# Kernel optimization log

Hardware: AMD Instinct MI355X
Metric: run time of the kernel (lower is better)

## Reference

```python
import jax, jax.numpy as jnp
import numpy as np

B, NPG, DEG = 512, 128, 16          # graphs, nodes/graph, out-degree
N = B * NPG                          # 65536 nodes
E = N * DEG                          # 1048576 edges
IN_DIM, HID, HEADS = 11, 32, 4
K1 = int(np.ceil(0.8 * NPG))         # 103 nodes/graph after pool1
K2 = int(np.ceil(0.8 * K1))          # 83 nodes/graph after pool2


def gat_conv(x, src, dst, mask, W, a_s, a_d, b, n_nodes):
    # PyG GATConv (concat=True, add_self_loops=True, eval mode -> no dropout)
    xp = (x @ W).reshape(n_nodes, HEADS, HID)            # [N,H,C]
    as_ = jnp.einsum('nhc,hc->nh', xp, a_s)
    ad_ = jnp.einsum('nhc,hc->nh', xp, a_d)
    loop = jnp.arange(n_nodes)
    s = jnp.concatenate([src, loop])
    d = jnp.concatenate([dst, loop])
    m = jnp.concatenate([mask, jnp.ones(n_nodes, bool)])
    logit = jax.nn.leaky_relu(as_[s] + ad_[d], 0.2)      # [E+N,H]
    logit = jnp.where(m[:, None], logit, -1e9)
    mx = jax.ops.segment_max(logit, d, num_segments=n_nodes)
    ex = jnp.exp(logit - mx[d]) * m[:, None]
    den = jax.ops.segment_sum(ex, d, num_segments=n_nodes)
    alpha = ex / (den[d] + 1e-16)                        # segment softmax over dst
    out = jax.ops.segment_sum(alpha[:, :, None] * xp[s], d, num_segments=n_nodes)
    return out.reshape(n_nodes, HEADS * HID) + b


def topk_pool(x, src, dst, mask, w, npg, k):
    # PyG TopKPooling: score = tanh((x*w).sum(-1)/||w||); keep top ceil(ratio*n) per graph
    nb = x.shape[0] // npg
    score = jnp.tanh((x @ w) / jnp.linalg.norm(w))
    vals, idx = jax.lax.top_k(score.reshape(nb, npg), k)  # [B,k]
    perm = (idx + (jnp.arange(nb) * npg)[:, None]).reshape(-1)
    x_new = x[perm] * vals.reshape(-1, 1)
    remap = jnp.full(nb * npg, -1).at[perm].set(jnp.arange(nb * k))
    ns, nd = remap[src], remap[dst]
    m = mask & (ns >= 0) & (nd >= 0)
    return x_new, jnp.where(m, ns, 0), jnp.where(m, nd, 0), m


def setup_inputs():
    key = jax.random.key(0)
    ks = jax.random.split(key, 24)
    s = 0.05
    x = jax.random.normal(ks[0], (N, IN_DIM), jnp.float32)
    src = jnp.repeat(jnp.arange(N), DEG)
    dst = (src // NPG) * NPG + jax.random.randint(ks[1], (E,), 0, NPG)
    edge_index = jnp.stack([src, dst])
    edge_attr = jax.random.normal(ks[2], (E, 4), jnp.float32)
    batch = jnp.repeat(jnp.arange(B), NPG)
    p = dict(
        W_g1=jax.random.normal(ks[3], (IN_DIM, HEADS * HID), jnp.float32) * s,
        att_src1=jax.random.normal(ks[4], (HEADS, HID), jnp.float32) * s,
        att_dst1=jax.random.normal(ks[5], (HEADS, HID), jnp.float32) * s,
        b_g1=jnp.zeros((HEADS * HID,), jnp.float32),
        W_t1=jax.random.normal(ks[6], (HEADS * HID, HID), jnp.float32) * s,
        b_t1=jnp.zeros((HID,), jnp.float32),
        pool_w1=jax.random.normal(ks[7], (HID,), jnp.float32) * s,
        W_g2=jax.random.normal(ks[8], (HID, HEADS * HID), jnp.float32) * s,
        att_src2=jax.random.normal(ks[9], (HEADS, HID), jnp.float32) * s,
        att_dst2=jax.random.normal(ks[10], (HEADS, HID), jnp.float32) * s,
        b_g2=jnp.zeros((HEADS * HID,), jnp.float32),
        W_t2=jax.random.normal(ks[11], (HEADS * HID, HID), jnp.float32) * s,
        b_t2=jnp.zeros((HID,), jnp.float32),
        pool_w2=jax.random.normal(ks[12], (HID,), jnp.float32) * s,
        W_l1=jax.random.normal(ks[13], (2 * HID, 256), jnp.float32) * s,
        b_l1=jnp.zeros((256,), jnp.float32),
        W_l2=jax.random.normal(ks[14], (256, 1024), jnp.float32) * s,
        b_l2=jnp.zeros((1024,), jnp.float32),
        W_l3=jax.random.normal(ks[15], (1024, 1), jnp.float32) * s,
        b_l3=jnp.zeros((1,), jnp.float32),
    )
    return dict(x=x, edge_index=edge_index, edge_attr=edge_attr, batch=batch, **p)


def reference(x, edge_index, edge_attr, batch,
              W_g1, att_src1, att_dst1, b_g1, W_t1, b_t1, pool_w1,
              W_g2, att_src2, att_dst2, b_g2, W_t2, b_t2, pool_w2,
              W_l1, b_l1, W_l2, b_l2, W_l3, b_l3):
    # edge_attr is ignored (GATConv built without edge_dim); batch is implicit
    # in the fixed equal-size graph layout.  Eval mode -> dropout disabled.
    src, dst = edge_index[0], edge_index[1]
    mask = jnp.ones(E, bool)
    h = jax.nn.relu(gat_conv(x, src, dst, mask, W_g1, att_src1, att_dst1, b_g1, N))
    h = h @ W_t1 + b_t1
    h, src, dst, mask = topk_pool(h, src, dst, mask, pool_w1, NPG, K1)
    h1 = h.reshape(B, K1, HID)
    g1 = jnp.concatenate([h1.max(1), h1.mean(1)], axis=1)   # [B, 2*HID]
    h = jax.nn.relu(gat_conv(h, src, dst, mask, W_g2, att_src2, att_dst2, b_g2, B * K1))
    h = h @ W_t2 + b_t2
    h, src, dst, mask = topk_pool(h, src, dst, mask, pool_w2, K1, K2)
    h2 = h.reshape(B, K2, HID)
    g2 = jnp.concatenate([h2.max(1), h2.mean(1)], axis=1)
    g = g1 + g2
    g = jax.nn.relu(g @ W_l1 + b_l1)
    g = jax.nn.relu(g @ W_l2 + b_l2)
    return g @ W_l3 + b_l3                                   # [B,1]
```

## Files before the change

### kernel.cpp

```cpp
#include <hip/hip_runtime.h>
#include <math.h>

constexpr int NPGc  = 128;
constexpr int NG    = 512;
constexpr int EPGc  = 2048;
constexpr int ETOT  = 1048576;
constexpr int IND   = 11;
constexpr int HIDc  = 32;
constexpr int FD    = 128;
constexpr int K1c   = 103;
constexpr int K2c   = 83;
constexpr int NN    = NG * NPGc;
constexpr int N2c   = NG * K1c;

__device__ __forceinline__ float lrelu(float x){ return fmaxf(x, 0.2f*x); }

template<int KIN>
__device__ void foldDev(const float* __restrict__ Wg, const float* __restrict__ avs,
                        const float* __restrict__ avd, float* __restrict__ S, float* __restrict__ D, int t)
{
    if (t < KIN * 4) {
        int k = t >> 2, h = t & 3;
        float s = 0.f, d = 0.f;
        for (int j = 0; j < HIDc; j++) {
            float w = Wg[k*FD + h*HIDc + j];
            s = fmaf(w, avs[h*HIDc + j], s);
            d = fmaf(w, avd[h*HIDc + j], d);
        }
        S[t] = s; D[t] = d;
    }
}

__global__ __launch_bounds__(256) void k_prep(const int* __restrict__ ei,
    const float* __restrict__ W1g, const float* __restrict__ s1, const float* __restrict__ d1,
    const float* __restrict__ W2g, const float* __restrict__ s2, const float* __restrict__ d2,
    int* __restrict__ csrOff, unsigned char* __restrict__ csrSB,
    float* __restrict__ S1, float* __restrict__ D1, float* __restrict__ S2, float* __restrict__ D2)
{
    int b = blockIdx.x, t = threadIdx.x;
    if (b >= NG) {
        if (b == NG)     foldDev<IND>(W1g, s1, d1, S1, D1, t);
        else             foldDev<HIDc>(W2g, s2, d2, S2, D2, t);
        return;
    }
    int g = b;
    __shared__ int cnt[128], cur[128], offL[129];
    __shared__ unsigned char sbL[EPGc];
    if (t < 128) cnt[t] = 0;
    __syncthreads();
    const int* dstG = ei + ETOT + g * EPGc;
    int dnv[8];
    #pragma unroll
    for (int q = 0; q < 8; q++) {
        int e = t + 256*q;
        dnv[q] = dstG[e] - g * NPGc;
        atomicAdd(&cnt[dnv[q]], 1);
    }
    __syncthreads();
    if (t < 64) {
        int c0 = cnt[2*t], c1 = cnt[2*t + 1], ps = c0 + c1, P = ps;
        #pragma unroll
        for (int dl = 1; dl < 64; dl <<= 1) { int v = __shfl_up(P, dl); if (t >= dl) P += v; }
        int E0 = P - ps;
        offL[2*t] = E0; offL[2*t + 1] = E0 + c0;
        cur[2*t]  = E0; cur[2*t + 1]  = E0 + c0;
        if (t == 63) offL[128] = P;
    }
    __syncthreads();
    #pragma unroll
    for (int q = 0; q < 8; q++) {
        int e = t + 256*q;
        int pos = atomicAdd(&cur[dnv[q]], 1);
        sbL[pos] = (unsigned char)(e >> 4);
    }
    __syncthreads();
    if (t < 128) ((int4*)(csrSB + (size_t)g * EPGc))[t] = ((const int4*)sbL)[t];
    if (t <= NPGc) csrOff[g*132 + t] = offL[t];
}

template<int NNODE, int KIN>
__global__ __launch_bounds__(256) void k_gat(
    const float* __restrict__ xin, const float* __restrict__ Wg,
    const float* __restrict__ WsS, const float* __restrict__ WsD,
    const int* __restrict__ csrOff, const unsigned char* __restrict__ csrSB,
    const float* __restrict__ bias, const float* __restrict__ Wt,
    float* __restrict__ htp)
{
    int g = blockIdx.x, h = blockIdx.y, t = threadIdx.x;
    constexpr int UN = (NNODE*KIN > EPGc ? NNODE*KIN : EPGc);
    __shared__ __align__(16) float xpL[NNODE * 36];
    __shared__ __align__(16) float uni[UN];
    __shared__ __align__(16) unsigned char sbL[EPGc];
    __shared__ float asL[NNODE], adL[NNODE], sfW[NNODE], sDen[NNODE];
    __shared__ int offL[NNODE + 1];
    __shared__ float WL[KIN * 32];
    __shared__ float WsSL[KIN], WsDL[KIN], bL[32];
    __shared__ __align__(16) float WtsL[1024];

    float* xF  = uni;
    float* wEL = uni;

    {
        const float* xg = xin + (size_t)g * NNODE * KIN;
        if constexpr ((KIN & 3) == 0) {
            for (int i = t; i < NNODE * (KIN/4); i += 256)
                ((float4*)xF)[i] = ((const float4*)xg)[i];
        } else {
            for (int i = t; i < NNODE * KIN; i += 256) xF[i] = xg[i];
        }
    }
    for (int i = t; i < KIN * 32; i += 256) { int k = i >> 5, c = i & 31; WL[i] = Wg[k*FD + h*32 + c]; }
    if (t < KIN) { WsSL[t] = WsS[t*4 + h]; WsDL[t] = WsD[t*4 + h]; }
    if (t < 32) bL[t] = bias[h*32 + t];
    if (t <= NNODE) offL[t] = csrOff[g*132 + t];
    if (t < 128) ((int4*)sbL)[t] = ((const int4*)(csrSB + (size_t)g * EPGc))[t];
    ((float4*)WtsL)[t] = ((const float4*)(Wt + h*1024))[t];
    __syncthreads();

    for (int p = t; p < NNODE * 32; p += 256) {
        int n = p >> 5, c = p & 31;
        const float* xr = xF + n * KIN;
        float acc = 0.f;
        #pragma unroll
        for (int k = 0; k < KIN; k++) acc = fmaf(xr[k], WL[k*32 + c], acc);
        xpL[n*36 + c] = acc;
    }
    if (t < NNODE) {
        const float* xr = xF + t * KIN;
        float s = 0.f, d = 0.f;
        #pragma unroll
        for (int k = 0; k < KIN; k++) { float v = xr[k]; s = fmaf(v, WsSL[k], s); d = fmaf(v, WsDL[k], d); }
        asL[t] = s; adL[t] = d;
    }
    __syncthreads();

    if (t < NNODE) {
        float as_n = asL[t], adn = adL[t];
        int lo = offL[t], hi = offL[t + 1];
        float mx = as_n;
        for (int i = lo; i < hi; i++) mx = fmaxf(mx, asL[sbL[i]]);
        float m = lrelu(mx + adn);
        float ws = expf(lrelu(as_n + adn) - m);
        float den = ws;
        for (int i = lo; i < hi; i++) {
            float w = expf(lrelu(asL[sbL[i]] + adn) - m);
            wEL[i] = w; den += w;
        }
        sfW[t] = ws; sDen[t] = den;
    }
    __syncthreads();

    const float4* X4 = (const float4*)xpL;
    float4 rv[4];
    #pragma unroll
    for (int r = 0; r < 4; r++) {
        int p = t + r*256;
        if (p < NNODE * 8) {
            int n = p >> 3, c4 = p & 7;
            float w0 = sfW[n];
            float4 v = X4[n*9 + c4];
            float4 a; a.x = w0*v.x; a.y = w0*v.y; a.z = w0*v.z; a.w = w0*v.w;
            int lo = offL[n], hi = offL[n + 1];
            for (int s = lo; s < hi; s++) {
                int sc = sbL[s]; float w = wEL[s];
                float4 u = X4[sc*9 + c4];
                a.x = fmaf(w, u.x, a.x); a.y = fmaf(w, u.y, a.y);
                a.z = fmaf(w, u.z, a.z); a.w = fmaf(w, u.w, a.w);
            }
            float inv = 1.f / (sDen[n] + 1e-16f);
            rv[r].x = fmaxf(fmaf(a.x, inv, bL[c4*4 + 0]), 0.f);
            rv[r].y = fmaxf(fmaf(a.y, inv, bL[c4*4 + 1]), 0.f);
            rv[r].z = fmaxf(fmaf(a.z, inv, bL[c4*4 + 2]), 0.f);
            rv[r].w = fmaxf(fmaf(a.w, inv, bL[c4*4 + 3]), 0.f);
        }
    }
    __syncthreads();
    {
        float4* X4w = (float4*)xpL;
        #pragma unroll
        for (int r = 0; r < 4; r++) {
            int p = t + r*256;
            if (p < NNODE * 8) X4w[(p>>3)*9 + (p&7)] = rv[r];
        }
    }
    __syncthreads();

    const int n0 = t >> 3, j4 = t & 7;
    float4 a0 = make_float4(0,0,0,0), a1 = a0, a2 = a0, a3 = a0;
    #pragma unroll 8
    for (int c = 0; c < 32; c++) {
        float4 w4 = *(const float4*)&WtsL[c*HIDc + j4*4];
        float r0 = xpL[n0*36 + c];
        a0.x = fmaf(r0, w4.x, a0.x); a0.y = fmaf(r0, w4.y, a0.y);
        a0.z = fmaf(r0, w4.z, a0.z); a0.w = fmaf(r0, w4.w, a0.w);
        if (n0 + 32 < NNODE) {
            float r1 = xpL[(n0+32)*36 + c];
            a1.x = fmaf(r1, w4.x, a1.x); a1.y = fmaf(r1, w4.y, a1.y);
            a1.z = fmaf(r1, w4.z, a1.z); a1.w = fmaf(r1, w4.w, a1.w);
        }
        if (n0 + 64 < NNODE) {
            float r2 = xpL[(n0+64)*36 + c];
            a2.x = fmaf(r2, w4.x, a2.x); a2.y = fmaf(r2, w4.y, a2.y);
            a2.z = fmaf(r2, w4.z, a2.z); a2.w = fmaf(r2, w4.w, a2.w);
        }
        if (n0 + 96 < NNODE) {
            float r3 = xpL[(n0+96)*36 + c];
            a3.x = fmaf(r3, w4.x, a3.x); a3.y = fmaf(r3, w4.y, a3.y);
            a3.z = fmaf(r3, w4.z, a3.z); a3.w = fmaf(r3, w4.w, a3.w);
        }
    }
    {
        size_t base = ((size_t)(g * NNODE + n0) * 4 + h) * 32 + j4 * 4;
        *(float4*)(htp + base) = a0;
        if (n0 + 32 < NNODE) *(float4*)(htp + base + (size_t)32*128) = a1;
        if (n0 + 64 < NNODE) *(float4*)(htp + base + (size_t)64*128) = a2;
        if (n0 + 96 < NNODE) *(float4*)(htp + base + (size_t)96*128) = a3;
    }
}

template<int NIN, int KEEP, bool FIRST>
__global__ __launch_bounds__(256) void k_linpool(
    const float* __restrict__ htp, const float* __restrict__ bt, const float* __restrict__ pw,
    float* __restrict__ xnew, const int* __restrict__ ei,
    int* __restrict__ csrOffW, unsigned char* __restrict__ sbW,
    float* __restrict__ gfeat, const float* __restrict__ gprev,
    const float* __restrict__ W1, const float* __restrict__ b1,
    const float* __restrict__ W2, const float* __restrict__ b2,
    const float* __restrict__ W3, const float* __restrict__ b3,
    float* __restrict__ outp)
{
    int g = blockIdx.x, t = threadIdx.x;
    __shared__ float htL[NIN * 33];
    __shared__ float scoreL[NIN];
    __shared__ int rnkL[NIN];
    __shared__ int cnt[128], cur[128], offL[129];
    __shared__ unsigned char sbL[EPGc];
    __shared__ float gvec[64];
    __shared__ float h1L[256], red[256];

    for (int p = t; p < NIN * 8; p += 256) {
        int n = p >> 3, q = p & 7;
        const float4* row = (const float4*)(htp + (size_t)(g * NIN + n) * 128);
        float4 s = ((const float4*)bt)[q];
        float4 p0 = row[q], p1 = row[8 + q], p2 = row[16 + q], p3 = row[24 + q];
        s.x += p0.x; s.y += p0.y; s.z += p0.z; s.w += p0.w;
        s.x += p1.x; s.y += p1.y; s.z += p1.z; s.w += p1.w;
        s.x += p2.x; s.y += p2.y; s.z += p2.z; s.w += p2.w;
        s.x += p3.x; s.y += p3.y; s.z += p3.z; s.w += p3.w;
        float* d = htL + n*33 + q*4;
        d[0] = s.x; d[1] = s.y; d[2] = s.z; d[3] = s.w;
    }
    __syncthreads();

    float nrm; { float ss = 0.f; for (int k = 0; k < HIDc; k++) { float w = pw[k]; ss = fmaf(w, w, ss); } nrm = sqrtf(ss); }
    if (t < NIN) {
        float dot = 0.f;
        for (int k = 0; k < HIDc; k++) dot = fmaf(htL[t*33 + k], pw[k], dot);
        scoreL[t] = tanhf(dot / nrm);
    }
    __syncthreads();
    if (t < NIN) {
        float si = scoreL[t]; int rank = 0;
        for (int q = 0; q < NIN; q++) {
            float sj = scoreL[q];
            rank += (sj > si || (sj == si && q < t)) ? 1 : 0;
        }
        rnkL[t] = (rank < KEEP) ? rank : -1;
    }
    __syncthreads();
    if constexpr (FIRST) {
        for (int p = t; p < NIN * 32; p += 256) {
            int n = p >> 5, jj = p & 31;
            int rk = rnkL[n];
            if (rk >= 0) xnew[((size_t)g*KEEP + rk)*HIDc + jj] = htL[n*33 + jj] * scoreL[n];
        }
    }
    if (t < HIDc) {
        float mx = -INFINITY, sm = 0.f;
        for (int n = 0; n < NIN; n++) {
            if (rnkL[n] >= 0) { float v = htL[n*33 + t] * scoreL[n]; mx = fmaxf(mx, v); sm += v; }
        }
        float mean = sm / (float)KEEP;
        if constexpr (FIRST) {
            gfeat[(size_t)g*64 + t]      = mx;
            gfeat[(size_t)g*64 + 32 + t] = mean;
        } else {
            gvec[t]      = gprev[(size_t)g*64 + t] + mx;
            gvec[32 + t] = gprev[(size_t)g*64 + 32 + t] + mean;
        }
    }

    if constexpr (FIRST) {
        __syncthreads();
        if (t < 128) cnt[t] = 0;
        __syncthreads();
        const int* dstG = ei + ETOT + g * EPGc;
        int snv[8], dnv[8];
        #pragma unroll
        for (int q = 0; q < 8; q++) {
            int e = t + 256*q;
            int s = rnkL[e >> 4], d = rnkL[dstG[e] - g * NPGc];
            bool ok = (s >= 0 && d >= 0);
            snv[q] = s; dnv[q] = ok ? d : -1;
            if (ok) atomicAdd(&cnt[d], 1);
        }
        __syncthreads();
        if (t < 64) {
            int c0 = cnt[2*t], c1 = cnt[2*t + 1], ps = c0 + c1, P = ps;
            #pragma unroll
            for (int dl = 1; dl < 64; dl <<= 1) { int v = __shfl_up(P, dl); if (t >= dl) P += v; }
            int E0 = P - ps;
            offL[2*t] = E0; offL[2*t + 1] = E0 + c0;
            cur[2*t]  = E0; cur[2*t + 1]  = E0 + c0;
            if (t == 63) offL[128] = P;
        }
        __syncthreads();
        #pragma unroll
        for (int q = 0; q < 8; q++) {
            if (dnv[q] >= 0) {
                int pos = atomicAdd(&cur[dnv[q]], 1);
                sbL[pos] = (unsigned char)snv[q];
            }
        }
        __syncthreads();
        if (t < 128) ((int4*)(sbW + (size_t)g * EPGc))[t] = ((const int4*)sbL)[t];
        if (t <= K1c) csrOffW[g*132 + t] = offL[t];
    } else {
        __syncthreads();
        float a = b1[t];
        #pragma unroll 4
        for (int k = 0; k < 64; k++) a = fmaf(gvec[k], W1[k*256 + t], a);
        h1L[t] = fmaxf(a, 0.f);
        __syncthreads();
        float c0 = b2[t], c1 = b2[t + 256], c2 = b2[t + 512], c3 = b2[t + 768];
        const float* w2c = W2 + t;
        #pragma unroll 4
        for (int i = 0; i < 256; i++) {
            float hv = h1L[i];
            const float* wr = w2c + (size_t)i * 1024;
            c0 = fmaf(hv, wr[0],   c0);
            c1 = fmaf(hv, wr[256], c1);
            c2 = fmaf(hv, wr[512], c2);
            c3 = fmaf(hv, wr[768], c3);
        }
        float p = fmaf(fmaxf(c0, 0.f), W3[t],
                  fmaf(fmaxf(c1, 0.f), W3[t + 256],
                  fmaf(fmaxf(c2, 0.f), W3[t + 512],
                       fmaxf(c3, 0.f) * W3[t + 768])));
        red[t] = p;
        __syncthreads();
        for (int s = 128; s > 0; s >>= 1) { if (t < s) red[t] += red[t + s]; __syncthreads(); }
        if (t == 0) outp[g] = red[0] + b3[0];
    }
}

extern "C" void kernel_launch(void* const* d_in, const int* in_sizes, int n_in,
                              void* d_out, int out_size, void* d_ws, size_t ws_size,
                              hipStream_t stream)
{
    const float* x    = (const float*)d_in[0];
    const int*   ei   = (const int*)  d_in[1];
    const float* W_g1 = (const float*)d_in[4];
    const float* as1w = (const float*)d_in[5];
    const float* ad1w = (const float*)d_in[6];
    const float* b_g1 = (const float*)d_in[7];
    const float* W_t1 = (const float*)d_in[8];
    const float* b_t1 = (const float*)d_in[9];
    const float* pw1  = (const float*)d_in[10];
    const float* W_g2 = (const float*)d_in[11];
    const float* as2w = (const float*)d_in[12];
    const float* ad2w = (const float*)d_in[13];
    const float* b_g2 = (const float*)d_in[14];
    const float* W_t2 = (const float*)d_in[15];
    const float* b_t2 = (const float*)d_in[16];
    const float* pw2  = (const float*)d_in[17];
    const float* W_l1 = (const float*)d_in[18];
    const float* b_l1 = (const float*)d_in[19];
    const float* W_l2 = (const float*)d_in[20];
    const float* b_l2 = (const float*)d_in[21];
    const float* W_l3 = (const float*)d_in[22];
    const float* b_l3 = (const float*)d_in[23];
    float* out = (float*)d_out;

    char* ws = (char*)d_ws;
    size_t off = 0;
    auto alloc = [&](size_t bytes) -> void* {
        void* p = (void*)(ws + off);
        off += ((bytes + 255) / 256) * 256;
        return p;
    };
    float* htp1  = (float*)alloc((size_t)NN * 128 * 4);
    float* htp2  = (float*)alloc((size_t)N2c * 128 * 4);
    float* x2    = (float*)alloc((size_t)N2c * HIDc * 4);
    float* g1    = (float*)alloc((size_t)NG * 64 * 4);
    float* wsS1  = (float*)alloc(64 * 4);
    float* wsD1  = (float*)alloc(64 * 4);
    float* wsS2  = (float*)alloc(128 * 4);
    float* wsD2  = (float*)alloc(128 * 4);
    int*   off1  = (int*)  alloc((size_t)NG * 132 * 4);
    unsigned char* sb1 = (unsigned char*)alloc((size_t)NG * EPGc);
    int*   off2  = (int*)  alloc((size_t)NG * 132 * 4);
    unsigned char* sb2 = (unsigned char*)alloc((size_t)NG * EPGc);

    k_prep<<<NG + 2, 256, 0, stream>>>(ei, W_g1, as1w, ad1w, W_g2, as2w, ad2w,
                                       off1, sb1, wsS1, wsD1, wsS2, wsD2);

    k_gat<NPGc, IND><<<dim3(NG, 4), 256, 0, stream>>>(
        x, W_g1, wsS1, wsD1, off1, sb1, b_g1, W_t1, htp1);

    k_linpool<NPGc, K1c, true><<<NG, 256, 0, stream>>>(
        htp1, b_t1, pw1, x2, ei, off2, sb2, g1, nullptr,
        nullptr, nullptr, nullptr, nullptr, nullptr, nullptr, nullptr);

    k_gat<K1c, HIDc><<<dim3(NG, 4), 256, 0, stream>>>(
        x2, W_g2, wsS2, wsD2, off2, sb2, b_g2, W_t2, htp2);

    k_linpool<K1c, K2c, false><<<NG, 256, 0, stream>>>(
        htp2, b_t2, pw2, nullptr, nullptr, nullptr, nullptr, nullptr, g1,
        W_l1, b_l1, W_l2, b_l2, W_l3, b_l3, out);
}
```

Baseline: 299.0 us.

## Pad CSR rows to 4, swizzle LDS features, and unroll GAT gathers

After: 622.7 us. 2.08x slower.

```diff
diff --git a/kernel.cpp b/kernel.cpp
--- a/kernel.cpp
+++ b/kernel.cpp
@@ -12,6 +12,9 @@
 constexpr int K2c   = 83;
 constexpr int NN    = NG * NPGc;
 constexpr int N2c   = NG * K1c;
+constexpr int EPAD  = 2432;
+constexpr int SBCAP = 2560;
+constexpr int OFFSTR= 264;
 
 __device__ __forceinline__ float lrelu(float x){ return fmaxf(x, 0.2f*x); }
 
@@ -45,8 +48,9 @@
     }
     int g = b;
     __shared__ int cnt[128], cur[128], offL[129];
-    __shared__ unsigned char sbL[EPGc];
+    __shared__ __align__(16) unsigned char sbL[SBCAP];
     if (t < 128) cnt[t] = 0;
+    if (t < SBCAP/16) ((int4*)sbL)[t] = make_int4(0,0,0,0);
     __syncthreads();
     const int* dstG = ei + ETOT + g * EPGc;
     int dnv[8];
@@ -58,12 +62,14 @@
     }
     __syncthreads();
     if (t < 64) {
-        int c0 = cnt[2*t], c1 = cnt[2*t + 1], ps = c0 + c1, P = ps;
+        int c0 = cnt[2*t], c1 = cnt[2*t + 1];
+        int p0 = (c0 + 3) & ~3, p1 = (c1 + 3) & ~3;
+        int ps = p0 + p1, P = ps;
         #pragma unroll
         for (int dl = 1; dl < 64; dl <<= 1) { int v = __shfl_up(P, dl); if (t >= dl) P += v; }
         int E0 = P - ps;
-        offL[2*t] = E0; offL[2*t + 1] = E0 + c0;
-        cur[2*t]  = E0; cur[2*t + 1]  = E0 + c0;
+        offL[2*t] = E0; offL[2*t + 1] = E0 + p0;
+        cur[2*t]  = E0; cur[2*t + 1]  = E0 + p0;
         if (t == 63) offL[128] = P;
     }
     __syncthreads();
@@ -74,12 +80,13 @@
         sbL[pos] = (unsigned char)(e >> 4);
     }
     __syncthreads();
-    if (t < 128) ((int4*)(csrSB + (size_t)g * EPGc))[t] = ((const int4*)sbL)[t];
-    if (t <= NPGc) csrOff[g*132 + t] = offL[t];
+    if (t < SBCAP/16) ((int4*)(csrSB + (size_t)g * SBCAP))[t] = ((const int4*)sbL)[t];
+    if (t <= 128) csrOff[g*OFFSTR + t] = offL[t];
+    if (t < 128)  csrOff[g*OFFSTR + 132 + t] = cur[t];
 }
 
 template<int NNODE, int KIN>
-__global__ __launch_bounds__(256) void k_gat(
+__global__ __launch_bounds__(256, 5) void k_gat(
     const float* __restrict__ xin, const float* __restrict__ Wg,
     const float* __restrict__ WsS, const float* __restrict__ WsD,
     const int* __restrict__ csrOff, const unsigned char* __restrict__ csrSB,
@@ -87,43 +94,45 @@
     float* __restrict__ htp)
 {
     int g = blockIdx.x, h = blockIdx.y, t = threadIdx.x;
-    constexpr int UN = (NNODE*KIN > EPGc ? NNODE*KIN : EPGc);
-    __shared__ __align__(16) float xpL[NNODE * 36];
+    constexpr int UN = (NNODE*KIN > EPAD ? NNODE*KIN : EPAD);
+    __shared__ __align__(16) float xpL[NNODE * 32];
     __shared__ __align__(16) float uni[UN];
-    __shared__ __align__(16) unsigned char sbL[EPGc];
+    __shared__ __align__(16) unsigned char sbL[SBCAP];
     __shared__ float asL[NNODE], adL[NNODE], sfW[NNODE], sDen[NNODE];
-    __shared__ int offL[NNODE + 1];
-    __shared__ float WL[KIN * 32];
+    __shared__ unsigned short offL[NNODE + 1], endL[NNODE];
     __shared__ float WsSL[KIN], WsDL[KIN], bL[32];
-    __shared__ __align__(16) float WtsL[1024];
 
     float* xF  = uni;
     float* wEL = uni;
 
+    float wcol[KIN];
+    {
+        const float* wg = Wg + h*32 + (t & 31);
+        #pragma unroll
+        for (int k = 0; k < KIN; k++) wcol[k] = wg[k*FD];
+    }
     {
         const float* xg = xin + (size_t)g * NNODE * KIN;
-        if constexpr ((KIN & 3) == 0) {
-            for (int i = t; i < NNODE * (KIN/4); i += 256)
-                ((float4*)xF)[i] = ((const float4*)xg)[i];
-        } else {
-            for (int i = t; i < NNODE * KIN; i += 256) xF[i] = xg[i];
-        }
-    }
-    for (int i = t; i < KIN * 32; i += 256) { int k = i >> 5, c = i & 31; WL[i] = Wg[k*FD + h*32 + c]; }
+        constexpr int XF4 = NNODE * KIN / 4;
+        for (int i = t; i < XF4; i += 256) ((float4*)xF)[i] = ((const float4*)xg)[i];
+    }
     if (t < KIN) { WsSL[t] = WsS[t*4 + h]; WsDL[t] = WsD[t*4 + h]; }
     if (t < 32) bL[t] = bias[h*32 + t];
-    if (t <= NNODE) offL[t] = csrOff[g*132 + t];
-    if (t < 128) ((int4*)sbL)[t] = ((const int4*)(csrSB + (size_t)g * EPGc))[t];
-    ((float4*)WtsL)[t] = ((const float4*)(Wt + h*1024))[t];
-    __syncthreads();
-
-    for (int p = t; p < NNODE * 32; p += 256) {
-        int n = p >> 5, c = p & 31;
-        const float* xr = xF + n * KIN;
-        float acc = 0.f;
-        #pragma unroll
-        for (int k = 0; k < KIN; k++) acc = fmaf(xr[k], WL[k*32 + c], acc);
-        xpL[n*36 + c] = acc;
+    if (t <= NNODE) offL[t] = (unsigned short)csrOff[g*OFFSTR + t];
+    if (t < NNODE)  endL[t] = (unsigned short)csrOff[g*OFFSTR + 132 + t];
+    if (t < SBCAP/16) ((int4*)sbL)[t] = ((const int4*)(csrSB + (size_t)g * SBCAP))[t];
+    __syncthreads();
+
+    {
+        const int c = t & 31, r0 = t >> 5;
+        const int c4v = c >> 2, csw = c & 3;
+        for (int r = r0; r < NNODE; r += 8) {
+            const float* xr = xF + r * KIN;
+            float acc = 0.f;
+            #pragma unroll
+            for (int k = 0; k < KIN; k++) acc = fmaf(xr[k], wcol[k], acc);
+            xpL[r*32 + (((c4v ^ (r & 7)) << 2) | csw)] = acc;
+        }
     }
     if (t < NNODE) {
         const float* xr = xF + t * KIN;
@@ -136,16 +145,34 @@
 
     if (t < NNODE) {
         float as_n = asL[t], adn = adL[t];
-        int lo = offL[t], hi = offL[t + 1];
+        int lo = offL[t], er = endL[t], hp = offL[t + 1];
         float mx = as_n;
-        for (int i = lo; i < hi; i++) mx = fmaxf(mx, asL[sbL[i]]);
+        int i = lo;
+        for (; i + 4 <= er; i += 4) {
+            unsigned int q4 = *(const unsigned int*)(sbL + i);
+            float a0 = asL[q4 & 255], a1 = asL[(q4 >> 8) & 255];
+            float a2 = asL[(q4 >> 16) & 255], a3 = asL[q4 >> 24];
+            mx = fmaxf(fmaxf(fmaxf(fmaxf(mx, a0), a1), a2), a3);
+        }
+        for (; i < er; i++) mx = fmaxf(mx, asL[sbL[i]]);
         float m = lrelu(mx + adn);
         float ws = expf(lrelu(as_n + adn) - m);
         float den = ws;
-        for (int i = lo; i < hi; i++) {
+        i = lo;
+        for (; i + 4 <= er; i += 4) {
+            unsigned int q4 = *(const unsigned int*)(sbL + i);
+            float w0 = expf(lrelu(asL[q4 & 255] + adn) - m);
+            float w1 = expf(lrelu(asL[(q4 >> 8) & 255] + adn) - m);
+            float w2 = expf(lrelu(asL[(q4 >> 16) & 255] + adn) - m);
+            float w3 = expf(lrelu(asL[q4 >> 24] + adn) - m);
+            *(float4*)(wEL + i) = make_float4(w0, w1, w2, w3);
+            den += w0; den += w1; den += w2; den += w3;
+        }
+        for (; i < er; i++) {
             float w = expf(lrelu(asL[sbL[i]] + adn) - m);
             wEL[i] = w; den += w;
         }
+        for (; i < hp; i++) wEL[i] = 0.f;
         sfW[t] = ws; sDen[t] = den;
     }
     __syncthreads();
@@ -158,14 +185,24 @@
         if (p < NNODE * 8) {
             int n = p >> 3, c4 = p & 7;
             float w0 = sfW[n];
-            float4 v = X4[n*9 + c4];
+            float4 v = X4[n*8 + (c4 ^ (n & 7))];
             float4 a; a.x = w0*v.x; a.y = w0*v.y; a.z = w0*v.z; a.w = w0*v.w;
             int lo = offL[n], hi = offL[n + 1];
-            for (int s = lo; s < hi; s++) {
-                int sc = sbL[s]; float w = wEL[s];
-                float4 u = X4[sc*9 + c4];
-                a.x = fmaf(w, u.x, a.x); a.y = fmaf(w, u.y, a.y);
-                a.z = fmaf(w, u.z, a.z); a.w = fmaf(w, u.w, a.w);
+            for (int s = lo; s < hi; s += 4) {
+                unsigned int q4 = *(const unsigned int*)(sbL + s);
+                float4 w4 = *(const float4*)(wEL + s);
+                int s0 = q4 & 255;         float4 u0 = X4[s0*8 + (c4 ^ (s0 & 7))];
+                a.x = fmaf(w4.x, u0.x, a.x); a.y = fmaf(w4.x, u0.y, a.y);
+                a.z = fmaf(w4.x, u0.z, a.z); a.w = fmaf(w4.x, u0.w, a.w);
+                int s1 = (q4 >> 8) & 255;  float4 u1 = X4[s1*8 + (c4 ^ (s1 & 7))];
+                a.x = fmaf(w4.y, u1.x, a.x); a.y = fmaf(w4.y, u1.y, a.y);
+                a.z = fmaf(w4.y, u1.z, a.z); a.w = fmaf(w4.y, u1.w, a.w);
+                int s2 = (q4 >> 16) & 255; float4 u2 = X4[s2*8 + (c4 ^ (s2 & 7))];
+                a.x = fmaf(w4.z, u2.x, a.x); a.y = fmaf(w4.z, u2.y, a.y);
+                a.z = fmaf(w4.z, u2.z, a.z); a.w = fmaf(w4.z, u2.w, a.w);
+                int s3 = q4 >> 24;         float4 u3 = X4[s3*8 + (c4 ^ (s3 & 7))];
+                a.x = fmaf(w4.w, u3.x, a.x); a.y = fmaf(w4.w, u3.y, a.y);
+                a.z = fmaf(w4.w, u3.z, a.z); a.w = fmaf(w4.w, u3.w, a.w);
             }
             float inv = 1.f / (sDen[n] + 1e-16f);
             rv[r].x = fmaxf(fmaf(a.x, inv, bL[c4*4 + 0]), 0.f);
@@ -180,33 +217,40 @@
         #pragma unroll
         for (int r = 0; r < 4; r++) {
             int p = t + r*256;
-            if (p < NNODE * 8) X4w[(p>>3)*9 + (p&7)] = rv[r];
+            if (p < NNODE * 8) {
+                int n = p >> 3, c4 = p & 7;
+                X4w[n*8 + (c4 ^ (n & 7))] = rv[r];
+            }
         }
     }
     __syncthreads();
 
     const int n0 = t >> 3, j4 = t & 7;
+    const float* WtH = Wt + h*1024 + j4*4;
     float4 a0 = make_float4(0,0,0,0), a1 = a0, a2 = a0, a3 = a0;
-    #pragma unroll 8
-    for (int c = 0; c < 32; c++) {
-        float4 w4 = *(const float4*)&WtsL[c*HIDc + j4*4];
-        float r0 = xpL[n0*36 + c];
-        a0.x = fmaf(r0, w4.x, a0.x); a0.y = fmaf(r0, w4.y, a0.y);
-        a0.z = fmaf(r0, w4.z, a0.z); a0.w = fmaf(r0, w4.w, a0.w);
-        if (n0 + 32 < NNODE) {
-            float r1 = xpL[(n0+32)*36 + c];
-            a1.x = fmaf(r1, w4.x, a1.x); a1.y = fmaf(r1, w4.y, a1.y);
-            a1.z = fmaf(r1, w4.z, a1.z); a1.w = fmaf(r1, w4.w, a1.w);
-        }
-        if (n0 + 64 < NNODE) {
-            float r2 = xpL[(n0+64)*36 + c];
-            a2.x = fmaf(r2, w4.x, a2.x); a2.y = fmaf(r2, w4.y, a2.y);
-            a2.z = fmaf(r2, w4.z, a2.z); a2.w = fmaf(r2, w4.w, a2.w);
-        }
-        if (n0 + 96 < NNODE) {
-            float r3 = xpL[(n0+96)*36 + c];
-            a3.x = fmaf(r3, w4.x, a3.x); a3.y = fmaf(r3, w4.y, a3.y);
-            a3.z = fmaf(r3, w4.z, a3.z); a3.w = fmaf(r3, w4.w, a3.w);
+    #pragma unroll
+    for (int c4 = 0; c4 < 8; c4++) {
+        const int sw = c4 ^ (n0 & 7);
+        float4 x0 = X4[n0*8 + sw];
+        float4 x1 = make_float4(0,0,0,0), x2v = x1, x3 = x1;
+        if (n0 + 32 < NNODE) x1  = X4[(n0+32)*8 + sw];
+        if (n0 + 64 < NNODE) x2v = X4[(n0+64)*8 + sw];
+        if (n0 + 96 < NNODE) x3  = X4[(n0+96)*8 + sw];
+        const float e0[4] = {x0.x, x0.y, x0.z, x0.w};
+        const float e1[4] = {x1.x, x1.y, x1.z, x1.w};
+        const float e2[4] = {x2v.x, x2v.y, x2v.z, x2v.w};
+        const float e3[4] = {x3.x, x3.y, x3.z, x3.w};
+        #pragma unroll
+        for (int j = 0; j < 4; j++) {
+            float4 w4 = *(const float4*)(WtH + (c4*4 + j)*32);
+            a0.x = fmaf(e0[j], w4.x, a0.x); a0.y = fmaf(e0[j], w4.y, a0.y);
+            a0.z = fmaf(e0[j], w4.z, a0.z); a0.w = fmaf(e0[j], w4.w, a0.w);
+            a1.x = fmaf(e1[j], w4.x, a1.x); a1.y = fmaf(e1[j], w4.y, a1.y);
+            a1.z = fmaf(e1[j], w4.z, a1.z); a1.w = fmaf(e1[j], w4.w, a1.w);
+            a2.x = fmaf(e2[j], w4.x, a2.x); a2.y = fmaf(e2[j], w4.y, a2.y);
+            a2.z = fmaf(e2[j], w4.z, a2.z); a2.w = fmaf(e2[j], w4.w, a2.w);
+            a3.x = fmaf(e3[j], w4.x, a3.x); a3.y = fmaf(e3[j], w4.y, a3.y);
+            a3.z = fmaf(e3[j], w4.z, a3.z); a3.w = fmaf(e3[j], w4.w, a3.w);
         }
     }
     {
@@ -234,7 +278,7 @@
     __shared__ float scoreL[NIN];
     __shared__ int rnkL[NIN];
     __shared__ int cnt[128], cur[128], offL[129];
-    __shared__ unsigned char sbL[EPGc];
+    __shared__ __align__(16) unsigned char sbL[SBCAP];
     __shared__ float gvec[64];
     __shared__ float h1L[256], red[256];
 
@@ -293,6 +337,7 @@
     if constexpr (FIRST) {
         __syncthreads();
         if (t < 128) cnt[t] = 0;
+        if (t < SBCAP/16) ((int4*)sbL)[t] = make_int4(0,0,0,0);
         __syncthreads();
         const int* dstG = ei + ETOT + g * EPGc;
         int snv[8], dnv[8];
@@ -306,12 +351,14 @@
         }
         __syncthreads();
         if (t < 64) {
-            int c0 = cnt[2*t], c1 = cnt[2*t + 1], ps = c0 + c1, P = ps;
+            int c0 = cnt[2*t], c1 = cnt[2*t + 1];
+            int p0 = (c0 + 3) & ~3, p1 = (c1 + 3) & ~3;
+            int ps = p0 + p1, P = ps;
             #pragma unroll
             for (int dl = 1; dl < 64; dl <<= 1) { int v = __shfl_up(P, dl); if (t >= dl) P += v; }
             int E0 = P - ps;
-            offL[2*t] = E0; offL[2*t + 1] = E0 + c0;
-            cur[2*t]  = E0; cur[2*t + 1]  = E0 + c0;
+            offL[2*t] = E0; offL[2*t + 1] = E0 + p0;
+            cur[2*t]  = E0; cur[2*t + 1]  = E0 + p0;
             if (t == 63) offL[128] = P;
         }
         __syncthreads();
@@ -323,8 +370,9 @@
             }
         }
         __syncthreads();
-        if (t < 128) ((int4*)(sbW + (size_t)g * EPGc))[t] = ((const int4*)sbL)[t];
-        if (t <= K1c) csrOffW[g*132 + t] = offL[t];
+        if (t < SBCAP/16) ((int4*)(sbW + (size_t)g * SBCAP))[t] = ((const int4*)sbL)[t];
+        if (t <= K1c) csrOffW[g*OFFSTR + t] = offL[t];
+        if (t < K1c)  csrOffW[g*OFFSTR + 132 + t] = cur[t];
     } else {
         __syncthreads();
         float a = b1[t];
@@ -397,10 +445,10 @@
     float* wsD1  = (float*)alloc(64 * 4);
     float* wsS2  = (float*)alloc(128 * 4);
     float* wsD2  = (float*)alloc(128 * 4);
-    int*   off1  = (int*)  alloc((size_t)NG * 132 * 4);
-    unsigned char* sb1 = (unsigned char*)alloc((size_t)NG * EPGc);
-    int*   off2  = (int*)  alloc((size_t)NG * 132 * 4);
-    unsigned char* sb2 = (unsigned char*)alloc((size_t)NG * EPGc);
+    int*   off1  = (int*)  alloc((size_t)NG * OFFSTR * 4);
+    unsigned char* sb1 = (unsigned char*)alloc((size_t)NG * SBCAP);
+    int*   off2  = (int*)  alloc((size_t)NG * OFFSTR * 4);
+    unsigned char* sb2 = (unsigned char*)alloc((size_t)NG * SBCAP);
 
     k_prep<<<NG + 2, 256, 0, stream>>>(ei, W_g1, as1w, ad1w, W_g2, as2w, ad2w,
                                        off1, sb1, wsS1, wsD1, wsS2, wsD2);
```
